# Optimization experiments

Hardware: AMD Instinct MI355X
Metric: run time of the kernel (lower is better)

## Reference

```python
import jax, jax.numpy as jnp
import numpy as np

B, T, C = 4, 2048, 1024
H = 16
D = C // H  # head_dim = 64


def setup_inputs() -> dict:
    key = jax.random.key(0)
    ks = jax.random.split(key, 9)
    s = 1.0 / np.sqrt(C)
    return {
        "x": jax.random.normal(ks[0], (B, T, C), dtype=jnp.float32),
        "Wk": jax.random.uniform(ks[1], (C, C), jnp.float32, -s, s),
        "bk": jax.random.uniform(ks[2], (C,), jnp.float32, -s, s),
        "Wq": jax.random.uniform(ks[3], (C, C), jnp.float32, -s, s),
        "bq": jax.random.uniform(ks[4], (C,), jnp.float32, -s, s),
        "Wv": jax.random.uniform(ks[5], (C, C), jnp.float32, -s, s),
        "bv": jax.random.uniform(ks[6], (C,), jnp.float32, -s, s),
        "Wp": jax.random.uniform(ks[7], (C, C), jnp.float32, -s, s),
        "bp": jax.random.uniform(ks[8], (C,), jnp.float32, -s, s),
    }


def reference(x, Wk, bk, Wq, bq, Wv, bv, Wp, bp):
    # projections -> (B, H, T, D)
    def split_heads(y):
        return y.reshape(B, T, H, D).transpose(0, 2, 1, 3)

    k = split_heads(x @ Wk.T + bk)
    q = split_heads(x @ Wq.T + bq)
    v = split_heads(x @ Wv.T + bv)

    att = jnp.einsum("bhtd,bhsd->bhts", q, k) / np.sqrt(D).astype(np.float32)
    causal = jnp.tril(jnp.ones((T, T), dtype=bool))
    att = jnp.where(causal, att, -jnp.inf)
    att = jax.nn.softmax(att, axis=-1)

    y = jnp.einsum("bhts,bhsd->bhtd", att, v)  # (B,H,T,D)
    y = y.transpose(0, 2, 1, 3).reshape(B, T, C)
    return y @ Wp.T + bp
```

## Files before the change

kernel.cpp:

```cpp
#include <hip/hip_runtime.h>
#include <hip/hip_bf16.h>

typedef unsigned short u16;
typedef unsigned int u32;
typedef short short8 __attribute__((ext_vector_type(8)));
typedef short short4v __attribute__((ext_vector_type(4)));
typedef float f32x4 __attribute__((ext_vector_type(4)));

#define MFMA16(a, b, c) __builtin_amdgcn_mfma_f32_16x16x32_bf16((a), (b), (c), 0, 0, 0)

constexpr int kB = 4, kT = 2048, kC = 1024, kH = 16, kD = 64;
constexpr int kBT = kB * kT;
constexpr long kQKV = (long)kB * kH * kT * kD;
constexpr float kSC = 0.125f * 1.4426950408889634f;

__device__ inline u16 f2bf(float f) {
    __hip_bfloat16 h = __float2bfloat16(f);
    return *reinterpret_cast<u16*>(&h);
}
__device__ inline u32 pkbf_trunc(float lo, float hi) {
    return __builtin_amdgcn_perm(__builtin_bit_cast(u32, hi),
                                 __builtin_bit_cast(u32, lo), 0x07060302u);
}
__device__ inline u32 pkbf_rne(float lo, float hi) {
    return ((u32)f2bf(hi) << 16) | (u32)f2bf(lo);
}

__device__ inline void cp16(const u16* g, u16* l) {
    __builtin_amdgcn_global_load_lds(
        (const __attribute__((address_space(1))) unsigned int*)g,
        (__attribute__((address_space(3))) unsigned int*)l, 16, 0, 0);
}

__global__ __launch_bounds__(256) void cast_kernel(
    const float* __restrict__ x,  const float* __restrict__ Wk,
    const float* __restrict__ Wq, const float* __restrict__ Wv,
    const float* __restrict__ Wp,
    u16* __restrict__ xb, u16* __restrict__ wkb, u16* __restrict__ wqb,
    u16* __restrict__ wvb, u16* __restrict__ wpb)
{
    const long id = (long)blockIdx.x * 256 + threadIdx.x;
    const float* src;
    u16* dst;
    long off;
    if (id < 2097152) {
        src = x; dst = xb; off = id;
    } else {
        const long w = (id - 2097152) >> 18;
        off = (id - 2097152) & 262143;
        src = (w == 0) ? Wk : (w == 1) ? Wq : (w == 2) ? Wv : Wp;
        dst = (w == 0) ? wkb : (w == 1) ? wqb : (w == 2) ? wvb : wpb;
    }
    f32x4 v = *(const f32x4*)&src[off * 4];
    short4v s = {(short)f2bf(v[0]), (short)f2bf(v[1]),
                 (short)f2bf(v[2]), (short)f2bf(v[3])};
    *(short4v*)&dst[off * 4] = s;
}

__global__ __launch_bounds__(256) void qkv_gemm_bf16(
    const u16* __restrict__ xb,
    const u16* __restrict__ wkb, const u16* __restrict__ wqb,
    const u16* __restrict__ wvb,
    const float* __restrict__ bk, const float* __restrict__ bq,
    const float* __restrict__ bv,
    u16* __restrict__ kw, u16* __restrict__ qw, u16* __restrict__ vw)
{
    __shared__ u16 As[128 * 32];
    __shared__ u16 Bs[128 * 32];
    const int tid = threadIdx.x;
    const int lane = tid & 63;
    const int wid = tid >> 6;
    const int l15 = lane & 15;
    const int quad = lane >> 4;
    const int m0 = blockIdx.x * 128;
    const int n0 = blockIdx.y * 128;
    const int z = blockIdx.z;

    const u16* W = (z == 0) ? wkb : (z == 1) ? wqb : wvb;
    const float* bias = (z == 0) ? bk : (z == 1) ? bq : bv;

    f32x4 zero = {0.f, 0.f, 0.f, 0.f};
    f32x4 acc[4][4];
#pragma unroll
    for (int i = 0; i < 4; ++i)
#pragma unroll
        for (int j = 0; j < 4; ++j) acc[i][j] = zero;

    const int wm = (wid & 1) * 64;
    const int wn = (wid >> 1) * 64;

    const int sRow = tid >> 2;
    const int sCol = (tid & 3) * 8;
    const int ldsOff = sRow * 32 + sCol;

    for (int k0 = 0; k0 < kC; k0 += 32) {
        cp16(&xb[(long)(m0 + sRow) * kC + k0 + sCol],      &As[ldsOff]);
        cp16(&xb[(long)(m0 + 64 + sRow) * kC + k0 + sCol], &As[64 * 32 + ldsOff]);
        cp16(&W[(long)(n0 + sRow) * kC + k0 + sCol],       &Bs[ldsOff]);
        cp16(&W[(long)(n0 + 64 + sRow) * kC + k0 + sCol],  &Bs[64 * 32 + ldsOff]);
        __syncthreads();
        short8 af[4], bfr[4];
#pragma unroll
        for (int mt = 0; mt < 4; ++mt)
            af[mt] = *(const short8*)&As[(wm + mt * 16 + l15) * 32 + quad * 8];
#pragma unroll
        for (int nt = 0; nt < 4; ++nt)
            bfr[nt] = *(const short8*)&Bs[(wn + nt * 16 + l15) * 32 + quad * 8];
#pragma unroll
        for (int mt = 0; mt < 4; ++mt)
#pragma unroll
            for (int nt = 0; nt < 4; ++nt)
                acc[mt][nt] = MFMA16(af[mt], bfr[nt], acc[mt][nt]);
        __syncthreads();
    }

    const float scale = (z == 1) ? kSC : 1.0f;
#pragma unroll
    for (int nt = 0; nt < 4; ++nt) {
        const int n = n0 + wn + nt * 16 + l15;
        const float bias_f = bias[n];
        const int h = n >> 6, d = n & 63;
#pragma unroll
        for (int mt = 0; mt < 4; ++mt) {
#pragma unroll
            for (int r = 0; r < 4; ++r) {
                const int m = m0 + wm + mt * 16 + quad * 4 + r;
                const int b = m >> 11, t = m & 2047;
                const float v = (acc[mt][nt][r] + bias_f) * scale;
                const int bh = b * kH + h;
                if (z == 2) {
                    vw[((long)bh * kD + d) * kT + t] = f2bf(v);
                } else {
                    u16* dst = (z == 0) ? kw : qw;
                    dst[((long)bh * kT + t) * kD + d] = f2bf(v);
                }
            }
        }
    }
}

__global__ __launch_bounds__(256) void qkv_gemm_kernel(
    const float* __restrict__ x,
    const float* __restrict__ Wk, const float* __restrict__ bk,
    const float* __restrict__ Wq, const float* __restrict__ bq,
    const float* __restrict__ Wv, const float* __restrict__ bv,
    u16* __restrict__ kw, u16* __restrict__ qw, u16* __restrict__ vw)
{
    __shared__ u16 As[128 * 32];
    __shared__ u16 Bs[128 * 32];
    const int tid = threadIdx.x;
    const int lane = tid & 63;
    const int wid = tid >> 6;
    const int l15 = lane & 15;
    const int quad = lane >> 4;
    const int m0 = blockIdx.x * 128;
    const int n0 = blockIdx.y * 128;
    const int z = blockIdx.z;

    const float* W = (z == 0) ? Wk : (z == 1) ? Wq : Wv;
    const float* bias = (z == 0) ? bk : (z == 1) ? bq : bv;

    f32x4 zero = {0.f, 0.f, 0.f, 0.f};
    f32x4 acc[4][4];
#pragma unroll
    for (int i = 0; i < 4; ++i)
#pragma unroll
        for (int j = 0; j < 4; ++j) acc[i][j] = zero;

    const int wm = (wid & 1) * 64;
    const int wn = (wid >> 1) * 64;
    const int row4 = tid >> 3;
    const int col4 = (tid & 7) * 4;

    for (int k0 = 0; k0 < kC; k0 += 32) {
#pragma unroll
        for (int p = 0; p < 4; ++p) {
            const int r = p * 32 + row4;
            f32x4 xa = *(const f32x4*)&x[(long)(m0 + r) * kC + k0 + col4];
            f32x4 wa = *(const f32x4*)&W[(long)(n0 + r) * kC + k0 + col4];
            short4v xs = {(short)f2bf(xa[0]), (short)f2bf(xa[1]),
                          (short)f2bf(xa[2]), (short)f2bf(xa[3])};
            short4v wsv = {(short)f2bf(wa[0]), (short)f2bf(wa[1]),
                           (short)f2bf(wa[2]), (short)f2bf(wa[3])};
            *(short4v*)&As[r * 32 + col4] = xs;
            *(short4v*)&Bs[r * 32 + col4] = wsv;
        }
        __syncthreads();
        short8 af[4], bfr[4];
#pragma unroll
        for (int mt = 0; mt < 4; ++mt)
            af[mt] = *(const short8*)&As[(wm + mt * 16 + l15) * 32 + quad * 8];
#pragma unroll
        for (int nt = 0; nt < 4; ++nt)
            bfr[nt] = *(const short8*)&Bs[(wn + nt * 16 + l15) * 32 + quad * 8];
#pragma unroll
        for (int mt = 0; mt < 4; ++mt)
#pragma unroll
            for (int nt = 0; nt < 4; ++nt)
                acc[mt][nt] = MFMA16(af[mt], bfr[nt], acc[mt][nt]);
        __syncthreads();
    }

    const float scale = (z == 1) ? kSC : 1.0f;
#pragma unroll
    for (int nt = 0; nt < 4; ++nt) {
        const int n = n0 + wn + nt * 16 + l15;
        const float bias_f = bias[n];
        const int h = n >> 6, d = n & 63;
#pragma unroll
        for (int mt = 0; mt < 4; ++mt) {
#pragma unroll
            for (int r = 0; r < 4; ++r) {
                const int m = m0 + wm + mt * 16 + quad * 4 + r;
                const int b = m >> 11, t = m & 2047;
                const float v = (acc[mt][nt][r] + bias_f) * scale;
                const int bh = b * kH + h;
                if (z == 2) {
                    vw[((long)bh * kD + d) * kT + t] = f2bf(v);
                } else {
                    u16* dst = (z == 0) ? kw : qw;
                    dst[((long)bh * kT + t) * kD + d] = f2bf(v);
                }
            }
        }
    }
}

__global__ __launch_bounds__(128, 2) void attn_kernel(
    const u16* qw, const u16* kw, const u16* vw, u16* ow)
{
    __shared__ u16 Ks[2][64 * 64];
    __shared__ u16 VT[2][64 * 64];
    __shared__ u16 Pb[64 * 64];

    const int tid = threadIdx.x;
    const int lane = tid & 63;
    const int wid = tid >> 6;
    const int l15 = lane & 15;
    const int quad = lane >> 4;
    const int id = blockIdx.x;
    const int bh = id & 63;
    const int pr = id >> 6;

    const float NEG = -1.0e30f;
    f32x4 zero = {0.f, 0.f, 0.f, 0.f};
    const short8 onesf = {(short)0x3F80, (short)0x3F80, (short)0x3F80, (short)0x3F80,
                          (short)0x3F80, (short)0x3F80, (short)0x3F80, (short)0x3F80};

    const int rl7 = l15 & 7;

    const u16* kbase = kw + (long)bh * kT * kD;
    const u16* vbase = vw + (long)bh * kD * kT;

    const u16* kp[4];
    const u16* vp[4];
#pragma unroll
    for (int q = 0; q < 4; ++q) {
        const int slot = q * 128 + tid;
        const int row = slot >> 3;
        const int c = slot & 7;
        const int off = (c ^ (row & 7)) * 8;
        kp[q] = kbase + (long)row * kD + off;
        vp[q] = vbase + (long)row * kT + off;
    }

    auto stage = [&](int buf, int st) {
        u16* kd = Ks[buf];
        u16* vd = VT[buf];
#pragma unroll
        for (int q = 0; q < 4; ++q) {
            cp16(kp[q] + (long)st * (64 * kD), kd + (q * 128 + tid) * 8);
            cp16(vp[q] + st * 64,              vd + (q * 128 + tid) * 8);
        }
    };

#pragma unroll
    for (int ph = 0; ph < 2; ++ph) {
        const int qt64 = ph ? (31 - pr) : pr;
        const int tw = qt64 * 64 + wid * 32;
        const int n_st = qt64 + 1;

        __syncthreads();
        stage(0, 0);

        short8 qf[2][2];
#pragma unroll
        for (int g = 0; g < 2; ++g) {
            const u16* qp = qw + ((long)bh * kT + tw + g * 16 + l15) * kD;
            qf[g][0] = *(const short8*)&qp[quad * 8];
            qf[g][1] = *(const short8*)&qp[32 + quad * 8];
        }

        f32x4 oacc[4][2];
#pragma unroll
        for (int mo = 0; mo < 4; ++mo)
#pragma unroll
            for (int g = 0; g < 2; ++g) oacc[mo][g] = zero;
        f32x4 lsum[2] = {zero, zero};

        for (int st = 0; st < n_st; ++st) {
            __syncthreads();
            const int cur = st & 1;
            if (st + 1 < n_st) stage(cur ^ 1, st + 1);

            const u16* K_ = Ks[cur];
            const u16* V_ = VT[cur];

            f32x4 sacc[4][2];
            __builtin_amdgcn_s_setprio(1);
#pragma unroll
            for (int ms = 0; ms < 4; ++ms) {
                const int row = ms * 16 + l15;
                short8 kf0 = *(const short8*)&K_[row * 64 + ((quad ^ rl7) * 8)];
                short8 kf1 = *(const short8*)&K_[row * 64 + (((4 + quad) ^ rl7) * 8)];
#pragma unroll
                for (int g = 0; g < 2; ++g) {
                    sacc[ms][g] = MFMA16(kf0, qf[g][0], zero);
                    sacc[ms][g] = MFMA16(kf1, qf[g][1], sacc[ms][g]);
                }
            }
            __builtin_amdgcn_s_setprio(0);

            if (st == n_st - 1) {
#pragma unroll
                for (int g = 0; g < 2; ++g) {
                    const int tl = wid * 32 + g * 16 + l15;
#pragma unroll
                    for (int ms = 0; ms < 4; ++ms)
#pragma unroll
                        for (int r = 0; r < 4; ++r)
                            if (ms * 16 + quad * 4 + r > tl) sacc[ms][g][r] = NEG;
                }
            }

#pragma unroll
            for (int g = 0; g < 2; ++g) {
                const int prow = wid * 32 + g * 16 + l15;
#pragma unroll
                for (int ms = 0; ms < 4; ++ms) {
                    const float p0 = exp2f(sacc[ms][g][0]);
                    const float p1 = exp2f(sacc[ms][g][1]);
                    const float p2 = exp2f(sacc[ms][g][2]);
                    const float p3 = exp2f(sacc[ms][g][3]);
                    uint2 pk;
                    pk.x = pkbf_trunc(p0, p1);
                    pk.y = pkbf_trunc(p2, p3);
                    const int chunk = (ms * 2 + (quad >> 1)) ^ rl7;
                    *(uint2*)&Pb[prow * 64 + chunk * 8 + (quad & 1) * 4] = pk;
                }
            }

            short8 pf[2][2];
#pragma unroll
            for (int g = 0; g < 2; ++g) {
                const int prow = wid * 32 + g * 16 + l15;
                pf[g][0] = *(const short8*)&Pb[prow * 64 + ((quad ^ rl7) * 8)];
                pf[g][1] = *(const short8*)&Pb[prow * 64 + (((4 + quad) ^ rl7) * 8)];
                lsum[g] = MFMA16(onesf, pf[g][0], lsum[g]);
                lsum[g] = MFMA16(onesf, pf[g][1], lsum[g]);
            }

            __builtin_amdgcn_s_setprio(1);
#pragma unroll
            for (int mo = 0; mo < 4; ++mo) {
                const int row = mo * 16 + l15;
                short8 vf0 = *(const short8*)&V_[row * 64 + ((quad ^ rl7) * 8)];
                short8 vf1 = *(const short8*)&V_[row * 64 + (((4 + quad) ^ rl7) * 8)];
#pragma unroll
                for (int g = 0; g < 2; ++g) {
                    oacc[mo][g] = MFMA16(vf0, pf[g][0], oacc[mo][g]);
                    oacc[mo][g] = MFMA16(vf1, pf[g][1], oacc[mo][g]);
                }
            }
            __builtin_amdgcn_s_setprio(0);
        }

#pragma unroll
        for (int g = 0; g < 2; ++g) {
            const float inv = 1.0f / lsum[g][0];
            const int t = tw + g * 16 + l15;
            u16* op = ow + ((long)bh * kT + t) * kD;
#pragma unroll
            for (int mo = 0; mo < 4; ++mo) {
                uint2 ov;
                ov.x = pkbf_rne(oacc[mo][g][0] * inv, oacc[mo][g][1] * inv);
                ov.y = pkbf_rne(oacc[mo][g][2] * inv, oacc[mo][g][3] * inv);
                *(uint2*)&op[mo * 16 + quad * 4] = ov;
            }
        }
    }
}

__global__ __launch_bounds__(256) void out_gemm_bf16(
    const u16* __restrict__ ob, const u16* __restrict__ wpb,
    const float* __restrict__ bp, float* __restrict__ out)
{
    __shared__ u16 As[128 * 32];
    __shared__ u16 Bs[128 * 32];
    const int tid = threadIdx.x;
    const int lane = tid & 63;
    const int wid = tid >> 6;
    const int l15 = lane & 15;
    const int quad = lane >> 4;
    const int m0 = blockIdx.x * 128;
    const int n0 = blockIdx.y * 128;

    f32x4 zero = {0.f, 0.f, 0.f, 0.f};
    f32x4 acc[4][4];
#pragma unroll
    for (int i = 0; i < 4; ++i)
#pragma unroll
        for (int j = 0; j < 4; ++j) acc[i][j] = zero;

    const int wm = (wid & 1) * 64;
    const int wn = (wid >> 1) * 64;

    const int sRow = tid >> 2;
    const int sCol = (tid & 3) * 8;
    const int ldsOff = sRow * 32 + sCol;

    for (int k0 = 0; k0 < kC; k0 += 32) {
        const int h = k0 >> 6;
        const int d = (k0 & 63) + sCol;
        {
            const int m = m0 + sRow, b = m >> 11, t = m & 2047;
            cp16(&ob[(((long)b * kH + h) * kT + t) * kD + d], &As[ldsOff]);
        }
        {
            const int m = m0 + 64 + sRow, b = m >> 11, t = m & 2047;
            cp16(&ob[(((long)b * kH + h) * kT + t) * kD + d], &As[64 * 32 + ldsOff]);
        }
        cp16(&wpb[(long)(n0 + sRow) * kC + k0 + sCol],      &Bs[ldsOff]);
        cp16(&wpb[(long)(n0 + 64 + sRow) * kC + k0 + sCol], &Bs[64 * 32 + ldsOff]);
        __syncthreads();
        short8 af[4], bfr[4];
#pragma unroll
        for (int mt = 0; mt < 4; ++mt)
            af[mt] = *(const short8*)&As[(wm + mt * 16 + l15) * 32 + quad * 8];
#pragma unroll
        for (int nt = 0; nt < 4; ++nt)
            bfr[nt] = *(const short8*)&Bs[(wn + nt * 16 + l15) * 32 + quad * 8];
#pragma unroll
        for (int mt = 0; mt < 4; ++mt)
#pragma unroll
            for (int nt = 0; nt < 4; ++nt)
                acc[mt][nt] = MFMA16(af[mt], bfr[nt], acc[mt][nt]);
        __syncthreads();
    }

#pragma unroll
    for (int nt = 0; nt < 4; ++nt) {
        const int n = n0 + wn + nt * 16 + l15;
        const float bias_f = bp[n];
#pragma unroll
        for (int mt = 0; mt < 4; ++mt) {
#pragma unroll
            for (int r = 0; r < 4; ++r) {
                const int m = m0 + wm + mt * 16 + quad * 4 + r;
                out[(long)m * kC + n] = acc[mt][nt][r] + bias_f;
            }
        }
    }
}

__global__ __launch_bounds__(256) void out_gemm_kernel(
    const u16* __restrict__ ow, const float* __restrict__ Wp,
    const float* __restrict__ bp, float* __restrict__ out)
{
    __shared__ u16 As[128 * 32];
    __shared__ u16 Bs[128 * 32];
    const int tid = threadIdx.x;
    const int lane = tid & 63;
    const int wid = tid >> 6;
    const int l15 = lane & 15;
    const int quad = lane >> 4;
    const int m0 = blockIdx.x * 128;
    const int n0 = blockIdx.y * 128;

    f32x4 zero = {0.f, 0.f, 0.f, 0.f};
    f32x4 acc[4][4];
#pragma unroll
    for (int i = 0; i < 4; ++i)
#pragma unroll
        for (int j = 0; j < 4; ++j) acc[i][j] = zero;

    const int wm = (wid & 1) * 64;
    const int wn = (wid >> 1) * 64;

    const int r0 = tid >> 2;
    const int kkA = (tid & 3) * 8;
    const int r1 = r0 + 64;
    const int row4 = tid >> 3;
    const int col4 = (tid & 7) * 4;

    for (int k0 = 0; k0 < kC; k0 += 32) {
        {
            const int m = m0 + r0, b = m >> 11, t = m & 2047;
            const int kk = k0 + kkA, h = kk >> 6, d = kk & 63;
            *(short8*)&As[r0 * 32 + kkA] =
                *(const short8*)&ow[(((long)b * kH + h) * kT + t) * kD + d];
        }
        {
            const int m = m0 + r1, b = m >> 11, t = m & 2047;
            const int kk = k0 + kkA, h = kk >> 6, d = kk & 63;
            *(short8*)&As[r1 * 32 + kkA] =
                *(const short8*)&ow[(((long)b * kH + h) * kT + t) * kD + d];
        }
#pragma unroll
        for (int p = 0; p < 4; ++p) {
            const int r = p * 32 + row4;
            f32x4 wa = *(const f32x4*)&Wp[(long)(n0 + r) * kC + k0 + col4];
            short4v wsv = {(short)f2bf(wa[0]), (short)f2bf(wa[1]),
                           (short)f2bf(wa[2]), (short)f2bf(wa[3])};
            *(short4v*)&Bs[r * 32 + col4] = wsv;
        }
        __syncthreads();
        short8 af[4], bfr[4];
#pragma unroll
        for (int mt = 0; mt < 4; ++mt)
            af[mt] = *(const short8*)&As[(wm + mt * 16 + l15) * 32 + quad * 8];
#pragma unroll
        for (int nt = 0; nt < 4; ++nt)
            bfr[nt] = *(const short8*)&Bs[(wn + nt * 16 + l15) * 32 + quad * 8];
#pragma unroll
        for (int mt = 0; mt < 4; ++mt)
#pragma unroll
            for (int nt = 0; nt < 4; ++nt)
                acc[mt][nt] = MFMA16(af[mt], bfr[nt], acc[mt][nt]);
        __syncthreads();
    }

#pragma unroll
    for (int nt = 0; nt < 4; ++nt) {
        const int n = n0 + wn + nt * 16 + l15;
        const float bias_f = bp[n];
#pragma unroll
        for (int mt = 0; mt < 4; ++mt) {
#pragma unroll
            for (int r = 0; r < 4; ++r) {
                const int m = m0 + wm + mt * 16 + quad * 4 + r;
                out[(long)m * kC + n] = acc[mt][nt][r] + bias_f;
            }
        }
    }
}

extern "C" void kernel_launch(void* const* d_in, const int* in_sizes, int n_in,
                              void* d_out, int out_size, void* d_ws, size_t ws_size,
                              hipStream_t stream) {
    const float* x  = (const float*)d_in[0];
    const float* Wk = (const float*)d_in[1];
    const float* bk = (const float*)d_in[2];
    const float* Wq = (const float*)d_in[3];
    const float* bq = (const float*)d_in[4];
    const float* Wv = (const float*)d_in[5];
    const float* bv = (const float*)d_in[6];
    const float* Wp = (const float*)d_in[7];
    const float* bp = (const float*)d_in[8];
    float* out = (float*)d_out;

    u16* ws = (u16*)d_ws;
    const size_t kNeed = 72ull * 1024 * 1024;

    if (ws_size >= kNeed) {
        u16* k_ws = ws;
        u16* q_ws = ws + kQKV;
        u16* v_ws = ws + 2 * kQKV;
        u16* xb   = ws + 3 * kQKV;
        u16* o_ws = xb;
        u16* wkb  = ws + 4 * kQKV;
        u16* wqb  = wkb + (long)kC * kC;
        u16* wvb  = wqb + (long)kC * kC;
        u16* wpb  = wvb + (long)kC * kC;

        cast_kernel<<<12288, 256, 0, stream>>>(x, Wk, Wq, Wv, Wp,
                                               xb, wkb, wqb, wvb, wpb);
        qkv_gemm_bf16<<<dim3(kBT / 128, kC / 128, 3), 256, 0, stream>>>(
            xb, wkb, wqb, wvb, bk, bq, bv, k_ws, q_ws, v_ws);
        attn_kernel<<<1024, 128, 0, stream>>>(q_ws, k_ws, v_ws, o_ws);
        out_gemm_bf16<<<dim3(kBT / 128, kC / 128), 256, 0, stream>>>(
            o_ws, wpb, bp, out);
    } else {
        u16* k_ws = ws;
        u16* q_ws = ws + kQKV;
        u16* v_ws = ws + 2 * kQKV;
        u16* o_ws = q_ws;

        qkv_gemm_kernel<<<dim3(kBT / 128, kC / 128, 3), 256, 0, stream>>>(
            x, Wk, bk, Wq, bq, Wv, bv, k_ws, q_ws, v_ws);
        attn_kernel<<<1024, 128, 0, stream>>>(q_ws, k_ws, v_ws, o_ws);
        out_gemm_kernel<<<dim3(kBT / 128, kC / 128), 256, 0, stream>>>(
            o_ws, Wp, bp, out);
    }
}
```

Baseline: 266.9 us.

## Double-buffer bf16 GEMMs with swizzled LDS, 128x256 tiles, 8 waves

Both bf16 projection GEMMs now use 512-thread blocks computing 128x256 tiles with K-step 64. Global-to-LDS copies go into a double-buffered, XOR-swizzled shared layout so the next tile loads while MFMAs run. Raw waitcnt, barriers and setprio split each step's MFMAs around the prefetch issue. This aims to hide load latency, cut LDS bank conflicts and halve syncs per K. In exchange it uses more LDS (96KB), runs one block per CU and launches half as many blocks.

```diff
diff --git a/kernel.cpp b/kernel.cpp
--- a/kernel.cpp
+++ b/kernel.cpp
@@ -57,7 +57,7 @@
     *(short4v*)&dst[off * 4] = s;
 }
 
-__global__ __launch_bounds__(256) void qkv_gemm_bf16(
+__global__ __launch_bounds__(512, 1) void qkv_gemm_bf16(
     const u16* __restrict__ xb,
     const u16* __restrict__ wkb, const u16* __restrict__ wqb,
     const u16* __restrict__ wvb,
@@ -65,15 +65,18 @@
     const float* __restrict__ bv,
     u16* __restrict__ kw, u16* __restrict__ qw, u16* __restrict__ vw)
 {
-    __shared__ u16 As[128 * 32];
-    __shared__ u16 Bs[128 * 32];
+    __shared__ u16 A2[2][128 * 64];
+    __shared__ u16 B2[2][256 * 64];
+
     const int tid = threadIdx.x;
     const int lane = tid & 63;
     const int wid = tid >> 6;
     const int l15 = lane & 15;
     const int quad = lane >> 4;
+    const int wr = wid & 1;
+    const int wc = wid >> 1;
     const int m0 = blockIdx.x * 128;
-    const int n0 = blockIdx.y * 128;
+    const int n0 = blockIdx.y * 256;
     const int z = blockIdx.z;
 
     const u16* W = (z == 0) ? wkb : (z == 1) ? wqb : wvb;
@@ -86,45 +89,110 @@
 #pragma unroll
         for (int j = 0; j < 4; ++j) acc[i][j] = zero;
 
-    const int wm = (wid & 1) * 64;
-    const int wn = (wid >> 1) * 64;
-
-    const int sRow = tid >> 2;
-    const int sCol = (tid & 3) * 8;
-    const int ldsOff = sRow * 32 + sCol;
-
-    for (int k0 = 0; k0 < kC; k0 += 32) {
-        cp16(&xb[(long)(m0 + sRow) * kC + k0 + sCol],      &As[ldsOff]);
-        cp16(&xb[(long)(m0 + 64 + sRow) * kC + k0 + sCol], &As[64 * 32 + ldsOff]);
-        cp16(&W[(long)(n0 + sRow) * kC + k0 + sCol],       &Bs[ldsOff]);
-        cp16(&W[(long)(n0 + 64 + sRow) * kC + k0 + sCol],  &Bs[64 * 32 + ldsOff]);
-        __syncthreads();
-        short8 af[4], bfr[4];
-#pragma unroll
-        for (int mt = 0; mt < 4; ++mt)
-            af[mt] = *(const short8*)&As[(wm + mt * 16 + l15) * 32 + quad * 8];
+    const u16* aSrc[2]; int aDst[2];
+#pragma unroll
+    for (int q = 0; q < 2; ++q) {
+        const int slot = q * 512 + tid;
+        const int row = slot >> 3, c = slot & 7;
+        aSrc[q] = xb + (long)(m0 + row) * kC + ((c ^ (row & 7)) * 8);
+        aDst[q] = slot * 8;
+    }
+    const u16* bSrc[4]; int bDst[4];
+#pragma unroll
+    for (int q = 0; q < 4; ++q) {
+        const int slot = q * 512 + tid;
+        const int row = slot >> 3, c = slot & 7;
+        bSrc[q] = W + (long)(n0 + row) * kC + ((c ^ (row & 7)) * 8);
+        bDst[q] = slot * 8;
+    }
+
+    auto stage = [&](int t, int cbuf) {
+        const long ko = (long)t * 64;
+#pragma unroll
+        for (int q = 0; q < 2; ++q) cp16(aSrc[q] + ko, &A2[cbuf][aDst[q]]);
+#pragma unroll
+        for (int q = 0; q < 4; ++q) cp16(bSrc[q] + ko, &B2[cbuf][bDst[q]]);
+    };
+
+    int aOff[4][2], bOff[4][2];
+#pragma unroll
+    for (int mt = 0; mt < 4; ++mt) {
+        const int row = wr * 64 + mt * 16 + l15;
+#pragma unroll
+        for (int k2 = 0; k2 < 2; ++k2)
+            aOff[mt][k2] = row * 64 + (((k2 * 4 + quad) ^ (row & 7)) * 8);
+    }
+#pragma unroll
+    for (int nt = 0; nt < 4; ++nt) {
+        const int row = wc * 64 + nt * 16 + l15;
+#pragma unroll
+        for (int k2 = 0; k2 < 2; ++k2)
+            bOff[nt][k2] = row * 64 + (((k2 * 4 + quad) ^ (row & 7)) * 8);
+    }
+
+    stage(0, 0);
+    stage(1, 1);
+    asm volatile("s_waitcnt vmcnt(6)" ::: "memory");
+    __builtin_amdgcn_s_barrier();
+
+    for (int t = 0; t < 16; ++t) {
+        const int c = t & 1;
+        short8 af[4][2], bf[4][2];
+#pragma unroll
+        for (int mt = 0; mt < 4; ++mt)
+#pragma unroll
+            for (int k2 = 0; k2 < 2; ++k2)
+                af[mt][k2] = *(const short8*)&A2[c][aOff[mt][k2]];
 #pragma unroll
         for (int nt = 0; nt < 4; ++nt)
-            bfr[nt] = *(const short8*)&Bs[(wn + nt * 16 + l15) * 32 + quad * 8];
-#pragma unroll
-        for (int mt = 0; mt < 4; ++mt)
-#pragma unroll
-            for (int nt = 0; nt < 4; ++nt)
-                acc[mt][nt] = MFMA16(af[mt], bfr[nt], acc[mt][nt]);
-        __syncthreads();
+#pragma unroll
+            for (int k2 = 0; k2 < 2; ++k2)
+                bf[nt][k2] = *(const short8*)&B2[c][bOff[nt][k2]];
+
+        __builtin_amdgcn_s_setprio(1);
+#pragma unroll
+        for (int mt = 0; mt < 4; ++mt)
+#pragma unroll
+            for (int nt = 0; nt < 2; ++nt) {
+                acc[mt][nt] = MFMA16(af[mt][0], bf[nt][0], acc[mt][nt]);
+                acc[mt][nt] = MFMA16(af[mt][1], bf[nt][1], acc[mt][nt]);
+            }
+        __builtin_amdgcn_s_setprio(0);
+
+        asm volatile("s_waitcnt lgkmcnt(0)" ::: "memory");
+        __builtin_amdgcn_s_barrier();
+
+        if (t + 2 < 16) stage(t + 2, c);
+
+        __builtin_amdgcn_s_setprio(1);
+#pragma unroll
+        for (int mt = 0; mt < 4; ++mt)
+#pragma unroll
+            for (int nt = 2; nt < 4; ++nt) {
+                acc[mt][nt] = MFMA16(af[mt][0], bf[nt][0], acc[mt][nt]);
+                acc[mt][nt] = MFMA16(af[mt][1], bf[nt][1], acc[mt][nt]);
+            }
+        __builtin_amdgcn_s_setprio(0);
+
+        if (t + 2 < 16) {
+            asm volatile("s_waitcnt vmcnt(6)" ::: "memory");
+        } else {
+            asm volatile("s_waitcnt vmcnt(0)" ::: "memory");
+        }
+        __builtin_amdgcn_s_barrier();
     }
 
     const float scale = (z == 1) ? kSC : 1.0f;
 #pragma unroll
     for (int nt = 0; nt < 4; ++nt) {
-        const int n = n0 + wn + nt * 16 + l15;
+        const int n = n0 + wc * 64 + nt * 16 + l15;
         const float bias_f = bias[n];
         const int h = n >> 6, d = n & 63;
 #pragma unroll
         for (int mt = 0; mt < 4; ++mt) {
 #pragma unroll
             for (int r = 0; r < 4; ++r) {
-                const int m = m0 + wm + mt * 16 + quad * 4 + r;
+                const int m = m0 + wr * 64 + mt * 16 + quad * 4 + r;
                 const int b = m >> 11, t = m & 2047;
                 const float v = (acc[mt][nt][r] + bias_f) * scale;
                 const int bh = b * kH + h;
@@ -391,19 +459,22 @@
     }
 }
 
-__global__ __launch_bounds__(256) void out_gemm_bf16(
+__global__ __launch_bounds__(512, 1) void out_gemm_bf16(
     const u16* __restrict__ ob, const u16* __restrict__ wpb,
     const float* __restrict__ bp, float* __restrict__ out)
 {
-    __shared__ u16 As[128 * 32];
-    __shared__ u16 Bs[128 * 32];
+    __shared__ u16 A2[2][128 * 64];
+    __shared__ u16 B2[2][256 * 64];
+
     const int tid = threadIdx.x;
     const int lane = tid & 63;
     const int wid = tid >> 6;
     const int l15 = lane & 15;
     const int quad = lane >> 4;
+    const int wr = wid & 1;
+    const int wc = wid >> 1;
     const int m0 = blockIdx.x * 128;
-    const int n0 = blockIdx.y * 128;
+    const int n0 = blockIdx.y * 256;
 
     f32x4 zero = {0.f, 0.f, 0.f, 0.f};
     f32x4 acc[4][4];
@@ -412,51 +483,110 @@
 #pragma unroll
         for (int j = 0; j < 4; ++j) acc[i][j] = zero;
 
-    const int wm = (wid & 1) * 64;
-    const int wn = (wid >> 1) * 64;
-
-    const int sRow = tid >> 2;
-    const int sCol = (tid & 3) * 8;
-    const int ldsOff = sRow * 32 + sCol;
-
-    for (int k0 = 0; k0 < kC; k0 += 32) {
-        const int h = k0 >> 6;
-        const int d = (k0 & 63) + sCol;
-        {
-            const int m = m0 + sRow, b = m >> 11, t = m & 2047;
-            cp16(&ob[(((long)b * kH + h) * kT + t) * kD + d], &As[ldsOff]);
-        }
-        {
-            const int m = m0 + 64 + sRow, b = m >> 11, t = m & 2047;
-            cp16(&ob[(((long)b * kH + h) * kT + t) * kD + d], &As[64 * 32 + ldsOff]);
-        }
-        cp16(&wpb[(long)(n0 + sRow) * kC + k0 + sCol],      &Bs[ldsOff]);
-        cp16(&wpb[(long)(n0 + 64 + sRow) * kC + k0 + sCol], &Bs[64 * 32 + ldsOff]);
-        __syncthreads();
-        short8 af[4], bfr[4];
-#pragma unroll
-        for (int mt = 0; mt < 4; ++mt)
-            af[mt] = *(const short8*)&As[(wm + mt * 16 + l15) * 32 + quad * 8];
+    const u16* aSrc[2]; int aDst[2];
+#pragma unroll
+    for (int q = 0; q < 2; ++q) {
+        const int slot = q * 512 + tid;
+        const int row = slot >> 3, c = slot & 7;
+        const int m = m0 + row, b = m >> 11, trow = m & 2047;
+        aSrc[q] = ob + (((long)b * kH) * kT + trow) * kD + ((c ^ (row & 7)) * 8);
+        aDst[q] = slot * 8;
+    }
+    const u16* bSrc[4]; int bDst[4];
+#pragma unroll
+    for (int q = 0; q < 4; ++q) {
+        const int slot = q * 512 + tid;
+        const int row = slot >> 3, c = slot & 7;
+        bSrc[q] = wpb + (long)(n0 + row) * kC + ((c ^ (row & 7)) * 8);
+        bDst[q] = slot * 8;
+    }
+
+    auto stage = [&](int t, int cbuf) {
+        const long koA = (long)t * kT * kD;
+        const long koB = (long)t * 64;
+#pragma unroll
+        for (int q = 0; q < 2; ++q) cp16(aSrc[q] + koA, &A2[cbuf][aDst[q]]);
+#pragma unroll
+        for (int q = 0; q < 4; ++q) cp16(bSrc[q] + koB, &B2[cbuf][bDst[q]]);
+    };
+
+    int aOff[4][2], bOff[4][2];
+#pragma unroll
+    for (int mt = 0; mt < 4; ++mt) {
+        const int row = wr * 64 + mt * 16 + l15;
+#pragma unroll
+        for (int k2 = 0; k2 < 2; ++k2)
+            aOff[mt][k2] = row * 64 + (((k2 * 4 + quad) ^ (row & 7)) * 8);
+    }
+#pragma unroll
+    for (int nt = 0; nt < 4; ++nt) {
+        const int row = wc * 64 + nt * 16 + l15;
+#pragma unroll
+        for (int k2 = 0; k2 < 2; ++k2)
+            bOff[nt][k2] = row * 64 + (((k2 * 4 + quad) ^ (row & 7)) * 8);
+    }
+
+    stage(0, 0);
+    stage(1, 1);
+    asm volatile("s_waitcnt vmcnt(6)" ::: "memory");
+    __builtin_amdgcn_s_barrier();
+
+    for (int t = 0; t < 16; ++t) {
+        const int c = t & 1;
+        short8 af[4][2], bf[4][2];
+#pragma unroll
+        for (int mt = 0; mt < 4; ++mt)
+#pragma unroll
+            for (int k2 = 0; k2 < 2; ++k2)
+                af[mt][k2] = *(const short8*)&A2[c][aOff[mt][k2]];
 #pragma unroll
         for (int nt = 0; nt < 4; ++nt)
-            bfr[nt] = *(const short8*)&Bs[(wn + nt * 16 + l15) * 32 + quad * 8];
-#pragma unroll
-        for (int mt = 0; mt < 4; ++mt)
-#pragma unroll
-            for (int nt = 0; nt < 4; ++nt)
-                acc[mt][nt] = MFMA16(af[mt], bfr[nt], acc[mt][nt]);
-        __syncthreads();
+#pragma unroll
+            for (int k2 = 0; k2 < 2; ++k2)
+                bf[nt][k2] = *(const short8*)&B2[c][bOff[nt][k2]];
+
+        __builtin_amdgcn_s_setprio(1);
+#pragma unroll
+        for (int mt = 0; mt < 4; ++mt)
+#pragma unroll
+            for (int nt = 0; nt < 2; ++nt) {
+                acc[mt][nt] = MFMA16(af[mt][0], bf[nt][0], acc[mt][nt]);
+                acc[mt][nt] = MFMA16(af[mt][1], bf[nt][1], acc[mt][nt]);
+            }
+        __builtin_amdgcn_s_setprio(0);
+
+        asm volatile("s_waitcnt lgkmcnt(0)" ::: "memory");
+        __builtin_amdgcn_s_barrier();
+
+        if (t + 2 < 16) stage(t + 2, c);
+
+        __builtin_amdgcn_s_setprio(1);
+#pragma unroll
+        for (int mt = 0; mt < 4; ++mt)
+#pragma unroll
+            for (int nt = 2; nt < 4; ++nt) {
+                acc[mt][nt] = MFMA16(af[mt][0], bf[nt][0], acc[mt][nt]);
+                acc[mt][nt] = MFMA16(af[mt][1], bf[nt][1], acc[mt][nt]);
+            }
+        __builtin_amdgcn_s_setprio(0);
+
+        if (t + 2 < 16) {
+            asm volatile("s_waitcnt vmcnt(6)" ::: "memory");
+        } else {
+            asm volatile("s_waitcnt vmcnt(0)" ::: "memory");
+        }
+        __builtin_amdgcn_s_barrier();
     }
 
 #pragma unroll
     for (int nt = 0; nt < 4; ++nt) {
-        const int n = n0 + wn + nt * 16 + l15;
+        const int n = n0 + wc * 64 + nt * 16 + l15;
         const float bias_f = bp[n];
 #pragma unroll
         for (int mt = 0; mt < 4; ++mt) {
 #pragma unroll
             for (int r = 0; r < 4; ++r) {
-                const int m = m0 + wm + mt * 16 + quad * 4 + r;
+                const int m = m0 + wr * 64 + mt * 16 + quad * 4 + r;
                 out[(long)m * kC + n] = acc[mt][nt][r] + bias_f;
             }
         }
@@ -575,10 +705,10 @@
 
         cast_kernel<<<12288, 256, 0, stream>>>(x, Wk, Wq, Wv, Wp,
                                                xb, wkb, wqb, wvb, wpb);
-        qkv_gemm_bf16<<<dim3(kBT / 128, kC / 128, 3), 256, 0, stream>>>(
+        qkv_gemm_bf16<<<dim3(kBT / 128, kC / 256, 3), 512, 0, stream>>>(
             xb, wkb, wqb, wvb, bk, bq, bv, k_ws, q_ws, v_ws);
         attn_kernel<<<1024, 128, 0, stream>>>(q_ws, k_ws, v_ws, o_ws);
-        out_gemm_bf16<<<dim3(kBT / 128, kC / 128), 256, 0, stream>>>(
+        out_gemm_bf16<<<dim3(kBT / 128, kC / 256), 512, 0, stream>>>(
             o_ws, wpb, bp, out);
     } else {
         u16* k_ws = ws;
```

New measurement: 266.8 us. About the same (-0.0%).
